# Performance work log

Hardware: AMD Instinct MI355X
Metric: run time of the kernel (lower is better)

Reference implementation:

```python
import jax, jax.numpy as jnp
import numpy as np

NH = 32          # nh * 2 neighbors per point (init nh=16)
P_REDUCTION = 0.5


def setup_inputs() -> dict:
    key = jax.random.key(0)
    k1, k2 = jax.random.split(key)
    x = jax.random.normal(k1, (2, 8192, 256), dtype=jnp.float32)       # [b, n, e]
    coords = jax.random.normal(k2, (2, 2, 8192, 1), dtype=jnp.float32) # [b, c, n, 1]
    return {"x": x, "coords": coords}


def _knn_gather(x, coords):
    """Return features of the NH nearest neighbors of each point: [b, n, NH, e]."""
    cs = coords[..., 0]                                   # [b, c, n]
    sq = jnp.sum(cs * cs, axis=1)                         # [b, n]
    # squared euclidean distances [b, n, n]
    d2 = sq[:, :, None] + sq[:, None, :] - 2.0 * jnp.einsum('bcn,bcm->bnm', cs, cs)
    d2 = jax.lax.stop_gradient(d2)                        # indices are non-differentiable
    _, nn_idx = jax.lax.top_k(-d2, NH)                    # [b, n, NH] nearest points
    # gather neighbor features: [b, 1, n, e] indexed with [b, n, NH, 1] -> [b, n, NH, e]
    x_nh = jnp.take_along_axis(x[:, None, :, :], nn_idx[..., None], axis=2)
    return x_nh


def _forward(x, coords):
    b, n, e = x.shape
    x_nh = _knn_gather(x, coords)                         # [b, n, NH, e]
    # unbiased std over the neighbor dim (torch.std default, ddof=1)
    mean_nh = jnp.mean(x_nh, axis=-2, keepdims=True)
    local_s = jnp.sqrt(jnp.sum((x_nh - mean_nh) ** 2, axis=-2) / (NH - 1))  # [b, n, e]
    global_m = jnp.abs(jnp.mean(x, axis=1))               # [b, e]
    local_dist = jnp.sum(local_s / global_m[:, None, :], axis=-1)           # [b, n]
    n_keep = int((1.0 - P_REDUCTION) * n)
    _, keep_idx = jax.lax.top_k(local_dist, n_keep)       # [b, n_keep], sorted desc
    x_out = jnp.take_along_axis(x, keep_idx[:, :, None], axis=1)            # [b, n_keep, e]
    coords_out = jnp.take_along_axis(coords, keep_idx[:, None, :, None], axis=2)  # [b, c, n_keep, 1]
    return x_out, coords_out, local_dist


def reference(x, coords):
    return _forward(x, coords)
```

## Files before the change

kernel.cpp:

```cpp
#include <hip/hip_runtime.h>

#define NN 8192
#define EE 256
#define KNH 32
#define NKEEP 4096
#define NCX 64
#define NCELL 4096
#define CNT_MIN 48

typedef unsigned long long u64;
typedef unsigned int u32;


__device__ __forceinline__ int cellof(float v) {
    const int q = (int)floorf((v + 4.6f) * (64.0f / 9.2f));
    return min(max(q, 0), NCX - 1);
}

__global__ void k_gm_partial(const float* __restrict__ x, const float* __restrict__ coords,
                             float* __restrict__ part, int* __restrict__ cellcnt) {
    const int b = blockIdx.y, chunk = blockIdx.x, t = threadIdx.x;
    const float* xp = x + ((size_t)b * NN + (size_t)chunk * 256) * EE + t;
    float s = 0.0f;
    for (int i = 0; i < 256; ++i) s += xp[(size_t)i * EE];
    part[((size_t)b * 32 + chunk) * EE + t] = s;

    const int i = chunk * 256 + t;
    const float xv = coords[(size_t)b * 2 * NN + i];
    const float yv = coords[(size_t)b * 2 * NN + NN + i];
    atomicAdd(&cellcnt[b * NCELL + cellof(xv) * NCX + cellof(yv)], 1);
}

__global__ void k_gm_final(const float* __restrict__ part, float* __restrict__ gm) {
    const int b = blockIdx.y, t = threadIdx.x;
    float s = 0.0f;
    for (int c = 0; c < 32; ++c) s += part[((size_t)b * 32 + c) * EE + t];
    gm[b * EE + t] = fabsf(s / (float)NN);
}

__global__ void k_cell_scan(const int* __restrict__ cellcnt, int* __restrict__ start,
                            int* __restrict__ fill) {
    __shared__ int ps[1024];
    const int b = blockIdx.x, t = threadIdx.x;
    int v0 = cellcnt[b * NCELL + t * 4 + 0];
    int v1 = cellcnt[b * NCELL + t * 4 + 1];
    int v2 = cellcnt[b * NCELL + t * 4 + 2];
    int v3 = cellcnt[b * NCELL + t * 4 + 3];
    const int s = v0 + v1 + v2 + v3;
    ps[t] = s;
    __syncthreads();
    for (int d = 1; d < 1024; d <<= 1) {
        const int add = (t >= d) ? ps[t - d] : 0;
        __syncthreads();
        ps[t] += add;
        __syncthreads();
    }
    int run = ps[t] - s;
    start[b * (NCELL + 1) + t * 4 + 0] = run; fill[b * NCELL + t * 4 + 0] = run; run += v0;
    start[b * (NCELL + 1) + t * 4 + 1] = run; fill[b * NCELL + t * 4 + 1] = run; run += v1;
    start[b * (NCELL + 1) + t * 4 + 2] = run; fill[b * NCELL + t * 4 + 2] = run; run += v2;
    start[b * (NCELL + 1) + t * 4 + 3] = run; fill[b * NCELL + t * 4 + 3] = run; run += v3;
    if (t == 1023) start[b * (NCELL + 1) + NCELL] = run;
}

__global__ void k_scatter(const float* __restrict__ coords, int* __restrict__ fill,
                          float2* __restrict__ sc, int* __restrict__ sj) {
    const int b = blockIdx.y;
    const int i = blockIdx.x * 256 + threadIdx.x;
    const float xv = coords[(size_t)b * 2 * NN + i];
    const float yv = coords[(size_t)b * 2 * NN + NN + i];
    const int p = atomicAdd(&fill[b * NCELL + cellof(xv) * NCX + cellof(yv)], 1);
    sc[(size_t)b * NN + p] = make_float2(xv, yv);
    sj[(size_t)b * NN + p] = i;
}

__device__ __forceinline__ u64 shfl_xor_u64(u64 v, int m) {
    const u32 hi = (u32)__shfl_xor((int)(u32)(v >> 32), m);
    const u32 lo = (u32)__shfl_xor((int)(u32)v, m);
    return ((u64)hi << 32) | lo;
}

__device__ __forceinline__ u64 wave_min_u64(u64 h) {
#pragma unroll
    for (int s = 1; s < 64; s <<= 1) {
        const u64 o = shfl_xor_u64(h, s);
        h = (o < h) ? o : h;
    }
    return h;
}

__global__ void __launch_bounds__(256) k_knn_dist(
        const float* __restrict__ x,
        const float* __restrict__ gm, const float2* __restrict__ sc,
        const int* __restrict__ sj, const int* __restrict__ start,
        float* __restrict__ ld_out) {
    __shared__ u64 comp[4][64];
    const int wg   = blockIdx.x;
    const int swz  = (wg & 7) * 512 + (wg >> 3);
    const int b    = swz >> 11;
    const int pb   = swz & 2047;
    const int wid  = threadIdx.x >> 6;
    const int lane = threadIdx.x & 63;
    const int p    = pb * 4 + wid;

    const float2* scb = sc + (size_t)b * NN;
    const int*    sjb = sj + (size_t)b * NN;
    const int*    stb = start + b * (NCELL + 1);
    const float2 cp = scb[p];
    const int    i  = sjb[p];
    const float ci0 = cp.x, ci1 = cp.y;
    const int qx = cellof(ci0), qy = cellof(ci1);

    int r = 1, xl, yl, yh, nsl;
    int myc0 = 0, mylen = 0;
    for (;;) {
        xl = max(qx - r, 0);
        const int xh = min(qx + r, NCX - 1);
        yl = max(qy - r, 0);
        yh = min(qy + r, NCX - 1);
        nsl = xh - xl + 1;
        int c0 = 0, c1 = 0;
        if (lane < nsl) {
            c0 = stb[(xl + lane) * NCX + yl];
            c1 = stb[(xl + lane) * NCX + yh + 1];
        }
        myc0 = c0; mylen = c1 - c0;
        int tot = mylen;
#pragma unroll
        for (int s = 1; s < 64; s <<= 1) tot += __shfl_xor(tot, s);
        if (tot >= CNT_MIN || r >= NCX) break;
        r <<= 1;
    }
    int incl = mylen;
#pragma unroll
    for (int d = 1; d < 64; d <<= 1) {
        const int v = __shfl_up(incl, d);
        incl += (lane >= d) ? v : 0;
    }
    int excl = incl - mylen;
    const int L1 = __shfl(incl, 63);

    float dmin = 1e30f;
    for (int g = 0; g < L1; g += 64) {
        const int gp = g + lane;
        int lo = 0, hi = nsl - 1;
#pragma unroll
        for (int st = 0; st < 6; ++st) {
            const int mid = (lo + hi + 1) >> 1;
            const int v = __shfl(excl, mid);
            const bool go = (v <= gp);
            lo = go ? mid : lo;
            hi = go ? hi : mid - 1;
        }
        const int cnd = __shfl(myc0, lo) + gp - __shfl(excl, lo);
        const int cc  = min(max(cnd, 0), NN - 1);
        const float2 pt = scb[cc];
        const float dx = ci0 - pt.x, dy = ci1 - pt.y;
        const float d  = fmaf(dx, dx, dy * dy);
        if (gp < L1) dmin = fminf(dmin, d);
    }

    u32 mk = __float_as_uint(dmin);
#pragma unroll
    for (int k = 2; k <= 64; k <<= 1) {
#pragma unroll
        for (int j = k >> 1; j > 0; j >>= 1) {
            const u32 o = (u32)__shfl_xor((int)mk, j);
            const bool keep_min = (((lane & j) == 0) == ((lane & k) == 0));
            const u32 mn = min(mk, o), mx = max(mk, o);
            mk = keep_min ? mn : mx;
        }
    }
    const u32 T = (u32)__shfl((int)mk, 31);

    const float srad = sqrtf(__uint_as_float(T)) * 1.0002f + 1e-5f;
    xl = cellof(ci0 - srad);
    const int xh2 = cellof(ci0 + srad);
    yl = cellof(ci1 - srad);
    yh = cellof(ci1 + srad);
    nsl = xh2 - xl + 1;
    {
        int c0 = 0, c1 = 0;
        if (lane < nsl) {
            c0 = stb[(xl + lane) * NCX + yl];
            c1 = stb[(xl + lane) * NCX + yh + 1];
        }
        myc0 = c0; mylen = c1 - c0;
    }
    incl = mylen;
#pragma unroll
    for (int d = 1; d < 64; d <<= 1) {
        const int v = __shfl_up(incl, d);
        incl += (lane >= d) ? v : 0;
    }
    excl = incl - mylen;
    const int L2 = __shfl(incl, 63);

    const u64 lmask = (1ull << lane) - 1;
    int base = 0;
    for (int g = 0; g < L2; g += 64) {
        const int gp = g + lane;
        int lo = 0, hi = nsl - 1;
#pragma unroll
        for (int st = 0; st < 6; ++st) {
            const int mid = (lo + hi + 1) >> 1;
            const int v = __shfl(excl, mid);
            const bool go = (v <= gp);
            lo = go ? mid : lo;
            hi = go ? hi : mid - 1;
        }
        const int cnd = __shfl(myc0, lo) + gp - __shfl(excl, lo);
        const int cc  = min(max(cnd, 0), NN - 1);
        const float2 pt = scb[cc];
        const int    jj = sjb[cc];
        const float dx = ci0 - pt.x, dy = ci1 - pt.y;
        const u32 db = __float_as_uint(fmaf(dx, dx, dy * dy));
        const bool keep = (gp < L2) && (db <= T);
        const u64 m = __ballot(keep);
        const int pos = base + __popcll(m & lmask);
        base += __popcll(m);
        if (keep && pos < 64) comp[wid][pos] = ((u64)db << 32) | (u32)jj;
    }
    const bool ovf = (base > 64) || (base < KNH);

    u64 key = (lane < base) ? comp[wid][lane] : ~0ull;
#pragma unroll
    for (int k = 2; k <= 64; k <<= 1) {
#pragma unroll
        for (int j = k >> 1; j > 0; j >>= 1) {
            const u64 other = shfl_xor_u64(key, j);
            const bool keep_min = (((lane & j) == 0) == ((lane & k) == 0));
            const bool lt = (key < other);
            const u64 mn = lt ? key : other;
            const u64 mx = lt ? other : key;
            key = keep_min ? mn : mx;
        }
    }
    int jkeep = (int)(u32)key;

    if (ovf) {
        u64 minkeep = 0;
        for (int k = 0; k < KNH; ++k) {
            u64 best = ~0ull;
            for (int g = 0; g < L2; g += 64) {
                const int gp = g + lane;
                int lo = 0, hi = nsl - 1;
#pragma unroll
                for (int st = 0; st < 6; ++st) {
                    const int mid = (lo + hi + 1) >> 1;
                    const int v = __shfl(excl, mid);
                    const bool go = (v <= gp);
                    lo = go ? mid : lo;
                    hi = go ? hi : mid - 1;
                }
                const int cnd = __shfl(myc0, lo) + gp - __shfl(excl, lo);
                const int cc  = min(max(cnd, 0), NN - 1);
                const float2 pt = scb[cc];
                const int    jj = sjb[cc];
                const float dx = ci0 - pt.x, dy = ci1 - pt.y;
                const float d  = fmaf(dx, dx, dy * dy);
                const u64 kk = ((u64)__float_as_uint(d) << 32) | (u32)jj;
                if (gp < L2 && kk >= minkeep && kk < best) best = kk;
            }
            const u64 h = wave_min_u64(best);
            if (lane == k) jkeep = (int)(u32)h;
            minkeep = h + 1;
        }
    }

    float s1[4] = {0.f, 0.f, 0.f, 0.f};
    float s2[4] = {0.f, 0.f, 0.f, 0.f};
    const float* xb = x + (size_t)b * NN * EE;
#pragma unroll 8
    for (int k = 0; k < KNH; ++k) {
        const int j = __shfl(jkeep, k);
        const float4 v = *reinterpret_cast<const float4*>(xb + (size_t)j * EE + (lane << 2));
        s1[0] += v.x; s2[0] += v.x * v.x;
        s1[1] += v.y; s2[1] += v.y * v.y;
        s1[2] += v.z; s2[2] += v.z * v.z;
        s1[3] += v.w; s2[3] += v.w * v.w;
    }

    const float* gmb = gm + b * EE;
    float tt = 0.f;
#pragma unroll
    for (int q = 0; q < 4; ++q) {
        const float sum = s1[q];
        float ssd = s2[q] - sum * sum * (1.0f / 32.0f);
        ssd = ssd > 0.f ? ssd : 0.f;
        const float ls = sqrtf(ssd * (1.0f / 31.0f));
        tt += ls / gmb[(lane << 2) + q];
    }
#pragma unroll
    for (int s2r = 1; s2r < 64; s2r <<= 1) tt += __shfl_xor(tt, s2r);

    if (lane == 0) ld_out[(size_t)b * NN + i] = tt;
}

__global__ void k_rank_gather(const float* __restrict__ x, const float* __restrict__ coords,
                              const float* __restrict__ ld,
                              float* __restrict__ x_out, float* __restrict__ c_out) {
    const int b    = blockIdx.y;
    const int wid  = threadIdx.x >> 6;
    const int lane = threadIdx.x & 63;
    const int i    = blockIdx.x * 4 + wid;
    const float* lb = ld + (size_t)b * NN;
    const float di = lb[i];
    int cnt = 0;
    for (int t = 0; t < NN / 64; ++t) {
        const int j = lane + t * 64;
        const float dj = lb[j];
        cnt += (dj > di || (dj == di && j < i)) ? 1 : 0;
    }
#pragma unroll
    for (int s = 1; s < 64; s <<= 1) cnt += __shfl_xor(cnt, s);

    if (cnt < NKEEP) {
        const float4 v = *reinterpret_cast<const float4*>(x + ((size_t)b * NN + i) * EE + (lane << 2));
        *reinterpret_cast<float4*>(x_out + ((size_t)b * NKEEP + cnt) * EE + (lane << 2)) = v;
        if (lane < 2) {
            c_out[((size_t)b * 2 + lane) * NKEEP + cnt] = coords[((size_t)b * 2 + lane) * NN + i];
        }
    }
}

extern "C" void kernel_launch(void* const* d_in, const int* in_sizes, int n_in,
                              void* d_out, int out_size, void* d_ws, size_t ws_size,
                              hipStream_t stream) {
    const float* x      = (const float*)d_in[0];
    const float* coords = (const float*)d_in[1];

    float* out    = (float*)d_out;
    float* x_out  = out;
    float* c_out  = out + 2097152;
    float* ld_out = out + 2113536;

    char*   ws      = (char*)d_ws;
    float*  part    = (float*)(ws);
    float*  gm      = (float*)(ws + 65536);
    int*    cellcnt = (int*)  (ws + 67584);
    int*    start   = (int*)  (ws + 100352);
    int*    fill    = (int*)  (ws + 133152);
    float2* sc      = (float2*)(ws + 165920);
    int*    sj      = (int*)  (ws + 296992);

    hipMemsetAsync(cellcnt, 0, 2 * NCELL * sizeof(int), stream);
    k_gm_partial <<<dim3(32, 2), 256,  0, stream>>>(x, coords, part, cellcnt);
    k_gm_final   <<<dim3(1, 2),  256,  0, stream>>>(part, gm);
    k_cell_scan  <<<2,           1024, 0, stream>>>(cellcnt, start, fill);
    k_scatter    <<<dim3(32, 2), 256,  0, stream>>>(coords, fill, sc, sj);
    k_knn_dist   <<<4096,        256,  0, stream>>>(x, gm, sc, sj, start, ld_out);
    k_rank_gather<<<dim3(2048, 2), 256, 0, stream>>>(x, coords, ld_out, x_out, c_out);
}
```

Before: 98.53 us.

## Fuse grid binning into a single shared-memory kernel and drop memset

Replaces the global-atomic cell counting, separate scan kernel, scatter kernel and memset with one kernel per batch that counts, scans and scatters points through shared-memory atomics. This removes two launches and a memset plus global atomic traffic, at the cost of doing the binning in only 2 blocks. The neighbor-index broadcast also switches from a shuffle to readlane, keeping it a scalar value.

New measurement: 99.04 us. Within noise of the previous version (+0.5%).

```diff
diff --git a/kernel.cpp b/kernel.cpp
--- a/kernel.cpp
+++ b/kernel.cpp
@@ -17,18 +17,12 @@
     return min(max(q, 0), NCX - 1);
 }
 
-__global__ void k_gm_partial(const float* __restrict__ x, const float* __restrict__ coords,
-                             float* __restrict__ part, int* __restrict__ cellcnt) {
+__global__ void k_gm_partial(const float* __restrict__ x, float* __restrict__ part) {
     const int b = blockIdx.y, chunk = blockIdx.x, t = threadIdx.x;
     const float* xp = x + ((size_t)b * NN + (size_t)chunk * 256) * EE + t;
     float s = 0.0f;
     for (int i = 0; i < 256; ++i) s += xp[(size_t)i * EE];
     part[((size_t)b * 32 + chunk) * EE + t] = s;
-
-    const int i = chunk * 256 + t;
-    const float xv = coords[(size_t)b * 2 * NN + i];
-    const float yv = coords[(size_t)b * 2 * NN + NN + i];
-    atomicAdd(&cellcnt[b * NCELL + cellof(xv) * NCX + cellof(yv)], 1);
 }
 
 __global__ void k_gm_final(const float* __restrict__ part, float* __restrict__ gm) {
@@ -38,14 +32,26 @@
     gm[b * EE + t] = fabsf(s / (float)NN);
 }
 
-__global__ void k_cell_scan(const int* __restrict__ cellcnt, int* __restrict__ start,
-                            int* __restrict__ fill) {
+__global__ void __launch_bounds__(1024) k_binning(const float* __restrict__ coords,
+                                                  int* __restrict__ start,
+                                                  float2* __restrict__ sc,
+                                                  int* __restrict__ sj) {
+    __shared__ int cnt[NCELL];
     __shared__ int ps[1024];
     const int b = blockIdx.x, t = threadIdx.x;
-    int v0 = cellcnt[b * NCELL + t * 4 + 0];
-    int v1 = cellcnt[b * NCELL + t * 4 + 1];
-    int v2 = cellcnt[b * NCELL + t * 4 + 2];
-    int v3 = cellcnt[b * NCELL + t * 4 + 3];
+#pragma unroll
+    for (int k = 0; k < 4; ++k) cnt[k * 1024 + t] = 0;
+    __syncthreads();
+#pragma unroll
+    for (int k = 0; k < 8; ++k) {
+        const int i = k * 1024 + t;
+        const float xv = coords[(size_t)b * 2 * NN + i];
+        const float yv = coords[(size_t)b * 2 * NN + NN + i];
+        atomicAdd(&cnt[cellof(xv) * NCX + cellof(yv)], 1);
+    }
+    __syncthreads();
+    const int v0 = cnt[t * 4 + 0], v1 = cnt[t * 4 + 1];
+    const int v2 = cnt[t * 4 + 2], v3 = cnt[t * 4 + 3];
     const int s = v0 + v1 + v2 + v3;
     ps[t] = s;
     __syncthreads();
@@ -56,22 +62,21 @@
         __syncthreads();
     }
     int run = ps[t] - s;
-    start[b * (NCELL + 1) + t * 4 + 0] = run; fill[b * NCELL + t * 4 + 0] = run; run += v0;
-    start[b * (NCELL + 1) + t * 4 + 1] = run; fill[b * NCELL + t * 4 + 1] = run; run += v1;
-    start[b * (NCELL + 1) + t * 4 + 2] = run; fill[b * NCELL + t * 4 + 2] = run; run += v2;
-    start[b * (NCELL + 1) + t * 4 + 3] = run; fill[b * NCELL + t * 4 + 3] = run; run += v3;
-    if (t == 1023) start[b * (NCELL + 1) + NCELL] = run;
-}
-
-__global__ void k_scatter(const float* __restrict__ coords, int* __restrict__ fill,
-                          float2* __restrict__ sc, int* __restrict__ sj) {
-    const int b = blockIdx.y;
-    const int i = blockIdx.x * 256 + threadIdx.x;
-    const float xv = coords[(size_t)b * 2 * NN + i];
-    const float yv = coords[(size_t)b * 2 * NN + NN + i];
-    const int p = atomicAdd(&fill[b * NCELL + cellof(xv) * NCX + cellof(yv)], 1);
-    sc[(size_t)b * NN + p] = make_float2(xv, yv);
-    sj[(size_t)b * NN + p] = i;
+    start[b * (NCELL + 1) + t * 4 + 0] = run; cnt[t * 4 + 0] = run; run += v0;
+    start[b * (NCELL + 1) + t * 4 + 1] = run; cnt[t * 4 + 1] = run; run += v1;
+    start[b * (NCELL + 1) + t * 4 + 2] = run; cnt[t * 4 + 2] = run; run += v2;
+    start[b * (NCELL + 1) + t * 4 + 3] = run; cnt[t * 4 + 3] = run; run += v3;
+    if (t == 0) start[b * (NCELL + 1) + NCELL] = NN;
+    __syncthreads();
+#pragma unroll
+    for (int k = 0; k < 8; ++k) {
+        const int i = k * 1024 + t;
+        const float xv = coords[(size_t)b * 2 * NN + i];
+        const float yv = coords[(size_t)b * 2 * NN + NN + i];
+        const int p = atomicAdd(&cnt[cellof(xv) * NCX + cellof(yv)], 1);
+        sc[(size_t)b * NN + p] = make_float2(xv, yv);
+        sj[(size_t)b * NN + p] = i;
+    }
 }
 
 __device__ __forceinline__ u64 shfl_xor_u64(u64 v, int m) {
@@ -273,7 +278,7 @@
     const float* xb = x + (size_t)b * NN * EE;
 #pragma unroll 8
     for (int k = 0; k < KNH; ++k) {
-        const int j = __shfl(jkeep, k);
+        const int j = __builtin_amdgcn_readlane(jkeep, k);
         const float4 v = *reinterpret_cast<const float4*>(xb + (size_t)j * EE + (lane << 2));
         s1[0] += v.x; s2[0] += v.x * v.x;
         s1[1] += v.y; s2[1] += v.y * v.y;
@@ -335,20 +340,16 @@
     float* c_out  = out + 2097152;
     float* ld_out = out + 2113536;
 
-    char*   ws      = (char*)d_ws;
-    float*  part    = (float*)(ws);
-    float*  gm      = (float*)(ws + 65536);
-    int*    cellcnt = (int*)  (ws + 67584);
-    int*    start   = (int*)  (ws + 100352);
-    int*    fill    = (int*)  (ws + 133152);
-    float2* sc      = (float2*)(ws + 165920);
-    int*    sj      = (int*)  (ws + 296992);
-
-    hipMemsetAsync(cellcnt, 0, 2 * NCELL * sizeof(int), stream);
-    k_gm_partial <<<dim3(32, 2), 256,  0, stream>>>(x, coords, part, cellcnt);
-    k_gm_final   <<<dim3(1, 2),  256,  0, stream>>>(part, gm);
-    k_cell_scan  <<<2,           1024, 0, stream>>>(cellcnt, start, fill);
-    k_scatter    <<<dim3(32, 2), 256,  0, stream>>>(coords, fill, sc, sj);
-    k_knn_dist   <<<4096,        256,  0, stream>>>(x, gm, sc, sj, start, ld_out);
-    k_rank_gather<<<dim3(2048, 2), 256, 0, stream>>>(x, coords, ld_out, x_out, c_out);
-}
+    char*   ws    = (char*)d_ws;
+    float*  part  = (float*)(ws);
+    float*  gm    = (float*)(ws + 65536);
+    int*    start = (int*)  (ws + 67584);
+    float2* sc    = (float2*)(ws + 100384);
+    int*    sj    = (int*)  (ws + 231456);
+
+    k_binning    <<<2,             1024, 0, stream>>>(coords, start, sc, sj);
+    k_gm_partial <<<dim3(32, 2),   256,  0, stream>>>(x, part);
+    k_gm_final   <<<dim3(1, 2),    256,  0, stream>>>(part, gm);
+    k_knn_dist   <<<4096,          256,  0, stream>>>(x, gm, sc, sj, start, ld_out);
+    k_rank_gather<<<dim3(2048, 2), 256,  0, stream>>>(x, coords, ld_out, x_out, c_out);
+}
```
